# Kernel tuning notes

Measured on AMD Instinct MI355X. Metric: run time of the kernel, lower is better.

## Reference

```python
import jax, jax.numpy as jnp
import numpy as np

N = 100000
E = 500000
D = 128      # input_dim
H = 4        # heads
C = 32       # per-head out channels (H*C == D)
HID = 512    # FFN hidden
EPS = 1e-5


def _layer_norm(x, w, b):
    mu = jnp.mean(x, axis=-1, keepdims=True)
    var = jnp.mean(jnp.square(x - mu), axis=-1, keepdims=True)
    return (x - mu) * jax.lax.rsqrt(var + EPS) * w + b


def setup_inputs() -> dict:
    key = jax.random.key(0)
    ks = jax.random.split(key, 16)
    s = 1.0 / np.sqrt(D)
    inp = {
        "x": jax.random.normal(ks[0], (N, D), dtype=jnp.float32),
        "edge_index": jax.random.randint(ks[1], (2, E), 0, N, dtype=jnp.int64),
        # TransformerConv params (lin_query/key/value/skip: D -> H*C == D)
        "Wq": jax.random.normal(ks[2], (D, D), dtype=jnp.float32) * s,
        "bq": jnp.zeros((D,), jnp.float32),
        "Wk": jax.random.normal(ks[3], (D, D), dtype=jnp.float32) * s,
        "bk": jnp.zeros((D,), jnp.float32),
        "Wv": jax.random.normal(ks[4], (D, D), dtype=jnp.float32) * s,
        "bv": jnp.zeros((D,), jnp.float32),
        "Wskip": jax.random.normal(ks[5], (D, D), dtype=jnp.float32) * s,
        "bskip": jnp.zeros((D,), jnp.float32),
        # lin_out
        "Wout": jax.random.normal(ks[6], (D, D), dtype=jnp.float32) * s,
        "bout": jnp.zeros((D,), jnp.float32),
        # LayerNorms
        "ln1_w": jnp.ones((D,), jnp.float32),
        "ln1_b": jnp.zeros((D,), jnp.float32),
        "ln2_w": jnp.ones((D,), jnp.float32),
        "ln2_b": jnp.zeros((D,), jnp.float32),
        # FFN
        "W1": jax.random.normal(ks[7], (HID, D), dtype=jnp.float32) * s,
        "b1": jnp.zeros((HID,), jnp.float32),
        "W2": jax.random.normal(ks[8], (D, HID), dtype=jnp.float32) * (1.0 / np.sqrt(HID)),
        "b2": jnp.zeros((D,), jnp.float32),
    }
    return inp


def _transformer_conv(x, src, dst, Wq, bq, Wk, bk, Wv, bv, Wskip, bskip):
    # q/k/v: [N, H, C]
    q = (x @ Wq.T + bq).reshape(N, H, C)
    k = (x @ Wk.T + bk).reshape(N, H, C)
    v = (x @ Wv.T + bv).reshape(N, H, C)
    # per-edge attention logits: [E, H]
    alpha = jnp.sum(q[dst] * k[src], axis=-1) / np.sqrt(C)
    # segment softmax over incoming edges of each destination node
    m = jax.ops.segment_max(alpha, dst, num_segments=N)       # [N, H]
    e = jnp.exp(alpha - m[dst])                               # [E, H]
    z = jax.ops.segment_sum(e, dst, num_segments=N)           # [N, H]
    a = e / z[dst]                                            # [E, H]
    # weighted aggregate of values: [N, H, C]
    msg = a[:, :, None] * v[src]
    out = jax.ops.segment_sum(msg, dst, num_segments=N)
    # root/skip connection (PyG root_weight=True)
    return out.reshape(N, H * C) + x @ Wskip.T + bskip


def reference(x, Wq, bq, Wk, bk, Wv, bv, Wskip, bskip, Wout, bout,
              ln1_w, ln1_b, W1, b1, W2, b2, ln2_w, ln2_b, edge_index):
    src = edge_index[0]
    dst = edge_index[1]
    conv = _transformer_conv(x, src, dst, Wq, bq, Wk, bk, Wv, bv, Wskip, bskip)
    out1 = conv @ Wout.T + bout
    out2 = _layer_norm(out1 + x, ln1_w, ln1_b)
    h = jax.nn.relu(out2 @ W1.T + b1)
    out3 = h @ W2.T + b2
    out4 = _layer_norm(out3 + out2, ln2_w, ln2_b)
    return out4
```

## Files before the change

### kernel.cpp

```cpp
#include <hip/hip_runtime.h>

#define NN   100000
#define NE   500000
#define DD   128
#define HH   4
#define HIDD 512
#define EPSF 1e-5f

typedef __bf16 bf16x8 __attribute__((ext_vector_type(8)));
typedef float  f32x4  __attribute__((ext_vector_type(4)));

__device__ __forceinline__ unsigned short f2b(float f) {
  unsigned u = __float_as_uint(f);
  unsigned r = (u + 0x7FFFu + ((u >> 16) & 1)) >> 16;
  return (unsigned short)r;
}
__device__ __forceinline__ float b2f(unsigned short s) {
  return __uint_as_float(((unsigned)s) << 16);
}

#define GLOAD16(ldsp, gp) __builtin_amdgcn_global_load_lds(                      \
    (const __attribute__((address_space(1))) void*)(gp),                         \
    (__attribute__((address_space(3))) void*)(ldsp), 16, 0, 0)

__device__ __forceinline__ void stageW(unsigned short* lds, const unsigned short* g,
                                       int ldg, int t) {
  const int w = t >> 6, l = t & 63;
#pragma unroll
  for (int i = 0; i < 8; i++) {
    const int chunk0 = i * 256 + w * 64;
    const int chunk = chunk0 + l;
    const int row = chunk >> 4, c16 = chunk & 15;
    const int gslot = c16 ^ (row & 15);
    GLOAD16(lds + (size_t)chunk0 * 8, g + (size_t)row * ldg + gslot * 8);
  }
}

__global__ void k_cast(const float* __restrict__ src, unsigned short* __restrict__ dst, int n) {
  int i = (blockIdx.x * 256 + threadIdx.x) * 4;
  if (i >= n) return;
  float4 v = *(const float4*)&src[i];
  ushort4 o;
  o.x = f2b(v.x); o.y = f2b(v.y); o.z = f2b(v.z); o.w = f2b(v.w);
  *(ushort4*)&dst[i] = o;
}

__global__ void k_castw(const float* __restrict__ Wq, const float* __restrict__ Wk,
                        const float* __restrict__ Wv, const float* __restrict__ Wsk,
                        const float* __restrict__ Wo, const float* __restrict__ W1,
                        const float* __restrict__ W2,
                        const float* __restrict__ bq, const float* __restrict__ bk,
                        const float* __restrict__ bv, const float* __restrict__ bs,
                        unsigned short* __restrict__ Wqkvs, unsigned short* __restrict__ Wob,
                        unsigned short* __restrict__ W1b, unsigned short* __restrict__ W2b,
                        float* __restrict__ bias512) {
  int i = blockIdx.x * 256 + threadIdx.x;
  if (i < 53248) {
    int e = i * 4;
    const float* src; unsigned short* dst; int off;
    if (e < 65536) {
      int seg = e >> 14;
      const float* s4[4] = {Wq, Wk, Wv, Wsk};
      src = s4[seg]; dst = Wqkvs + (seg << 14); off = e & 16383;
    } else if (e < 81920) { src = Wo;  dst = Wob; off = e - 65536; }
    else if (e < 147456)  { src = W1;  dst = W1b; off = e - 81920; }
    else                  { src = W2;  dst = W2b; off = e - 147456; }
    float4 v = *(const float4*)&src[off];
    ushort4 o; o.x = f2b(v.x); o.y = f2b(v.y); o.z = f2b(v.z); o.w = f2b(v.w);
    *(ushort4*)&dst[off] = o;
  } else if (i < 53376) {
    int b4 = (i - 53248) * 4;
    const float* srcs[4] = {bq, bk, bv, bs};
#pragma unroll
    for (int j = 0; j < 4; j++) {
      int idx = b4 + j;
      bias512[idx] = srcs[idx >> 7][idx & 127];
    }
  }
}

__global__ void k_zero_cnt(int* __restrict__ cnt) {
  int i = blockIdx.x * 256 + threadIdx.x;
  if (i < NN) cnt[i] = 0;
}
__global__ void k_count(const int* __restrict__ ei, int* __restrict__ cnt) {
  int e = blockIdx.x * 256 + threadIdx.x;
  if (e < NE) atomicAdd(&cnt[ei[NE + e]], 1);
}
__global__ void k_scan1(const int* __restrict__ cnt, int* __restrict__ rowptr, int* __restrict__ part) {
  __shared__ int sh[256];
  int i = blockIdx.x * 256 + threadIdx.x;
  int v = (i < NN) ? cnt[i] : 0;
  sh[threadIdx.x] = v; __syncthreads();
  for (int off = 1; off < 256; off <<= 1) {
    int t = (threadIdx.x >= off) ? sh[threadIdx.x - off] : 0;
    __syncthreads();
    sh[threadIdx.x] += t;
    __syncthreads();
  }
  if (i < NN) rowptr[i] = sh[threadIdx.x] - v;
  if (threadIdx.x == 255) part[blockIdx.x] = sh[255];
}
__global__ void k_scan2(const int* __restrict__ part, int* __restrict__ partx) {
  __shared__ int sh[512];
  int t = threadIdx.x;
  int v = (t < 391) ? part[t] : 0;
  sh[t] = v; __syncthreads();
  for (int off = 1; off < 512; off <<= 1) {
    int u = (t >= off) ? sh[t - off] : 0;
    __syncthreads();
    sh[t] += u;
    __syncthreads();
  }
  partx[t] = sh[t] - v;
}
__global__ void k_scan3(int* __restrict__ rowptr, const int* __restrict__ partx, int* __restrict__ cnt) {
  int i = blockIdx.x * 256 + threadIdx.x;
  if (i < NN) {
    int r = rowptr[i] + partx[i >> 8];
    rowptr[i] = r;
    cnt[i] = r;
  }
  if (i == 0) rowptr[NN] = NE;
}
__global__ void k_scatter(const int* __restrict__ ei, int* __restrict__ cnt, int* __restrict__ csr_src) {
  int e = blockIdx.x * 256 + threadIdx.x;
  if (e >= NE) return;
  int d = ei[NE + e];
  int pos = atomicAdd(&cnt[d], 1);
  csr_src[pos] = ei[e];
}

#define LOADA(dst, Aptr, LDA_, kb)                                               \
  _Pragma("unroll") for (int ks = 0; ks < 4; ks++)                               \
    _Pragma("unroll") for (int rt = 0; rt < 2; rt++) {                           \
      const int row_ = n0 + rt * 16 + lq;                                        \
      bf16x8 zz = {};                                                            \
      dst[ks][rt] = (row_ < NN)                                                  \
          ? *(const bf16x8*)&(Aptr)[(size_t)row_ * (LDA_) + (kb) + ks * 32 + hq * 8] \
          : zz;                                                                  \
    }

__global__ __launch_bounds__(256, 2) void k_gemm_cg(const unsigned short* __restrict__ A,
                                                    const unsigned short* __restrict__ W,
                                                    const float* __restrict__ bias,
                                                    unsigned short* __restrict__ outB) {
  __shared__ __align__(16) unsigned short Ws[128 * 128];
  const int t = threadIdx.x;
  const int w = t >> 6, l = t & 63;
  const int n0 = blockIdx.x * 128 + w * 32;
  const int lq = l & 15, hq = l >> 4;

  bf16x8 af[4][2];
  LOADA(af, A, 128, 0);
#pragma unroll 1
  for (int cg = 0; cg < 4; ++cg) {
    if (cg) __syncthreads();
    stageW(Ws, W + (size_t)cg * 128 * 128, 128, t);
    __syncthreads();
    f32x4 acc[2][8] = {};
#pragma unroll
    for (int ks = 0; ks < 4; ks++) {
      bf16x8 b[8];
      const int c16 = ks * 4 + hq;
#pragma unroll
      for (int ct = 0; ct < 8; ct++) {
        const int row = ct * 16 + lq;
        b[ct] = *(const bf16x8*)&Ws[row * 128 + ((c16 ^ lq) * 8)];
      }
#pragma unroll
      for (int rt = 0; rt < 2; rt++)
#pragma unroll
        for (int ct = 0; ct < 8; ct++)
          acc[rt][ct] = __builtin_amdgcn_mfma_f32_16x16x32_bf16(b[ct], af[ks][rt], acc[rt][ct], 0, 0, 0);
    }
#pragma unroll
    for (int rt = 0; rt < 2; rt++) {
      const int row = n0 + rt * 16 + lq;
      if (row < NN) {
#pragma unroll
        for (int ct = 0; ct < 8; ct++) {
          const int col = cg * 128 + ct * 16 + hq * 4;
          const float4 bs = *(const float4*)&bias[col];
          ushort4 o;
          o.x = f2b(acc[rt][ct][0] + bs.x);
          o.y = f2b(acc[rt][ct][1] + bs.y);
          o.z = f2b(acc[rt][ct][2] + bs.z);
          o.w = f2b(acc[rt][ct][3] + bs.w);
          *(ushort4*)&outB[(size_t)row * 512 + col] = o;
        }
      }
    }
  }
}

__global__ __launch_bounds__(256, 4) void k_gemm_ln1(const unsigned short* __restrict__ A,
                                                     const unsigned short* __restrict__ W,
                                                     const float* __restrict__ bias,
                                                     const unsigned short* __restrict__ resB,
                                                     const float* __restrict__ lw,
                                                     const float* __restrict__ lb,
                                                     unsigned short* __restrict__ outB) {
  __shared__ __align__(16) unsigned short Ws[128 * 128];
  const int t = threadIdx.x;
  const int w = t >> 6, l = t & 63;
  const int n0 = blockIdx.x * 128 + w * 32;
  const int lq = l & 15, hq = l >> 4;

  bf16x8 af[4][2];
  LOADA(af, A, 512, 0);
  stageW(Ws, W, 128, t);
  __syncthreads();
  f32x4 acc[2][8] = {};
#pragma unroll
  for (int ks = 0; ks < 4; ks++) {
    bf16x8 b[8];
    const int c16 = ks * 4 + hq;
#pragma unroll
    for (int ct = 0; ct < 8; ct++) {
      const int row = ct * 16 + lq;
      b[ct] = *(const bf16x8*)&Ws[row * 128 + ((c16 ^ lq) * 8)];
    }
#pragma unroll
    for (int rt = 0; rt < 2; rt++)
#pragma unroll
      for (int ct = 0; ct < 8; ct++)
        acc[rt][ct] = __builtin_amdgcn_mfma_f32_16x16x32_bf16(b[ct], af[ks][rt], acc[rt][ct], 0, 0, 0);
  }
#pragma unroll
  for (int rt = 0; rt < 2; rt++) {
    const int row = n0 + rt * 16 + lq;
#pragma unroll
    for (int ct = 0; ct < 8; ct++) {
      const int col = ct * 16 + hq * 4;
      const float4 bs = *(const float4*)&bias[col];
      ushort4 rv = make_ushort4(0, 0, 0, 0);
      if (row < NN) rv = *(const ushort4*)&resB[(size_t)row * DD + col];
      acc[rt][ct][0] += bs.x + b2f(rv.x);
      acc[rt][ct][1] += bs.y + b2f(rv.y);
      acc[rt][ct][2] += bs.z + b2f(rv.z);
      acc[rt][ct][3] += bs.w + b2f(rv.w);
    }
    float s = 0.f;
#pragma unroll
    for (int ct = 0; ct < 8; ct++)
#pragma unroll
      for (int j = 0; j < 4; j++) s += acc[rt][ct][j];
    s += __shfl_xor(s, 16, 64); s += __shfl_xor(s, 32, 64);
    const float mu = s * (1.f / 128.f);
    float vs = 0.f;
#pragma unroll
    for (int ct = 0; ct < 8; ct++)
#pragma unroll
      for (int j = 0; j < 4; j++) { float d = acc[rt][ct][j] - mu; vs += d * d; }
    vs += __shfl_xor(vs, 16, 64); vs += __shfl_xor(vs, 32, 64);
    const float rs = rsqrtf(vs * (1.f / 128.f) + EPSF);
    if (row < NN) {
#pragma unroll
      for (int ct = 0; ct < 8; ct++) {
        const int col = ct * 16 + hq * 4;
        const float4 lw4 = *(const float4*)&lw[col];
        const float4 lb4 = *(const float4*)&lb[col];
        ushort4 o;
        o.x = f2b((acc[rt][ct][0] - mu) * rs * lw4.x + lb4.x);
        o.y = f2b((acc[rt][ct][1] - mu) * rs * lw4.y + lb4.y);
        o.z = f2b((acc[rt][ct][2] - mu) * rs * lw4.z + lb4.z);
        o.w = f2b((acc[rt][ct][3] - mu) * rs * lw4.w + lb4.w);
        *(ushort4*)&outB[(size_t)row * DD + col] = o;
      }
    }
  }
}

__global__ __launch_bounds__(256, 2) void k_ffn_fused(const unsigned short* __restrict__ A,
                                                      const unsigned short* __restrict__ W1,
                                                      const float* __restrict__ b1,
                                                      const unsigned short* __restrict__ W2,
                                                      const float* __restrict__ b2,
                                                      const float* __restrict__ lw,
                                                      const float* __restrict__ lb,
                                                      float* __restrict__ outF) {
  __shared__ __align__(16) unsigned short Ws[128 * 128];
  __shared__ __align__(16) unsigned short Hs[128 * 128];
  const int t = threadIdx.x;
  const int w = t >> 6, l = t & 63;
  const int n0 = blockIdx.x * 128 + w * 32;
  const int lq = l & 15, hq = l >> 4;
  const int lrow = w * 32;

  bf16x8 af[4][2];
  LOADA(af, A, 128, 0);

  f32x4 acc2[2][8] = {};
#pragma unroll 1
  for (int cg = 0; cg < 4; ++cg) {
    if (cg) __syncthreads();
    stageW(Ws, W1 + (size_t)cg * 128 * 128, 128, t);
    __syncthreads();
    f32x4 acc1[2][8] = {};
#pragma unroll
    for (int ks = 0; ks < 4; ks++) {
      bf16x8 b[8];
      const int c16 = ks * 4 + hq;
#pragma unroll
      for (int ct = 0; ct < 8; ct++) {
        const int row = ct * 16 + lq;
        b[ct] = *(const bf16x8*)&Ws[row * 128 + ((c16 ^ lq) * 8)];
      }
#pragma unroll
      for (int rt = 0; rt < 2; rt++)
#pragma unroll
        for (int ct = 0; ct < 8; ct++)
          acc1[rt][ct] = __builtin_amdgcn_mfma_f32_16x16x32_bf16(b[ct], af[ks][rt], acc1[rt][ct], 0, 0, 0);
    }
#pragma unroll
    for (int rt = 0; rt < 2; rt++) {
      const int row = lrow + rt * 16 + lq;
#pragma unroll
      for (int ct = 0; ct < 8; ct++) {
        const int col = ct * 16 + hq * 4;
        const float4 bs = *(const float4*)&b1[cg * 128 + col];
        ushort4 o;
        o.x = f2b(fmaxf(acc1[rt][ct][0] + bs.x, 0.f));
        o.y = f2b(fmaxf(acc1[rt][ct][1] + bs.y, 0.f));
        o.z = f2b(fmaxf(acc1[rt][ct][2] + bs.z, 0.f));
        o.w = f2b(fmaxf(acc1[rt][ct][3] + bs.w, 0.f));
        *(ushort4*)&Hs[row * 128 + (((col >> 3) ^ lq) * 8) + (col & 7)] = o;
      }
    }
    __syncthreads();
    stageW(Ws, W2 + (size_t)cg * 128, 512, t);
    __syncthreads();
#pragma unroll
    for (int ks = 0; ks < 4; ks++) {
      bf16x8 b[8];
      const int c16 = ks * 4 + hq;
#pragma unroll
      for (int ct = 0; ct < 8; ct++) {
        const int row = ct * 16 + lq;
        b[ct] = *(const bf16x8*)&Ws[row * 128 + ((c16 ^ lq) * 8)];
      }
      bf16x8 h[2];
#pragma unroll
      for (int rt = 0; rt < 2; rt++) {
        const int row = lrow + rt * 16 + lq;
        h[rt] = *(const bf16x8*)&Hs[row * 128 + (((ks * 4 + hq) ^ lq) * 8)];
      }
#pragma unroll
      for (int rt = 0; rt < 2; rt++)
#pragma unroll
        for (int ct = 0; ct < 8; ct++)
          acc2[rt][ct] = __builtin_amdgcn_mfma_f32_16x16x32_bf16(b[ct], h[rt], acc2[rt][ct], 0, 0, 0);
    }
  }

#pragma unroll
  for (int rt = 0; rt < 2; rt++) {
    const int row = n0 + rt * 16 + lq;
#pragma unroll
    for (int ct = 0; ct < 8; ct++) {
      const int col = ct * 16 + hq * 4;
      const float4 bs = *(const float4*)&b2[col];
      ushort4 rv = make_ushort4(0, 0, 0, 0);
      if (row < NN) rv = *(const ushort4*)&A[(size_t)row * DD + col];
      acc2[rt][ct][0] += bs.x + b2f(rv.x);
      acc2[rt][ct][1] += bs.y + b2f(rv.y);
      acc2[rt][ct][2] += bs.z + b2f(rv.z);
      acc2[rt][ct][3] += bs.w + b2f(rv.w);
    }
    float s = 0.f;
#pragma unroll
    for (int ct = 0; ct < 8; ct++)
#pragma unroll
      for (int j = 0; j < 4; j++) s += acc2[rt][ct][j];
    s += __shfl_xor(s, 16, 64); s += __shfl_xor(s, 32, 64);
    const float mu = s * (1.f / 128.f);
    float vs = 0.f;
#pragma unroll
    for (int ct = 0; ct < 8; ct++)
#pragma unroll
      for (int j = 0; j < 4; j++) { float d = acc2[rt][ct][j] - mu; vs += d * d; }
    vs += __shfl_xor(vs, 16, 64); vs += __shfl_xor(vs, 32, 64);
    const float rs = rsqrtf(vs * (1.f / 128.f) + EPSF);
    if (row < NN) {
#pragma unroll
      for (int ct = 0; ct < 8; ct++) {
        const int col = ct * 16 + hq * 4;
        const float4 lw4 = *(const float4*)&lw[col];
        const float4 lb4 = *(const float4*)&lb[col];
        float4 o;
        o.x = (acc2[rt][ct][0] - mu) * rs * lw4.x + lb4.x;
        o.y = (acc2[rt][ct][1] - mu) * rs * lw4.y + lb4.y;
        o.z = (acc2[rt][ct][2] - mu) * rs * lw4.z + lb4.z;
        o.w = (acc2[rt][ct][3] - mu) * rs * lw4.w + lb4.w;
        *(float4*)&outF[(size_t)row * DD + col] = o;
      }
    }
  }
}

__global__ __launch_bounds__(256) void k_attn(const int* __restrict__ csr_src,
                                              const int* __restrict__ rowptr,
                                              unsigned short* qkvsb) {
  const int l = threadIdx.x & 31;
  const int node = blockIdx.x * 8 + (threadIdx.x >> 5);
  const int row0 = rowptr[node], row1 = rowptr[node + 1];
  ushort4 qu = *(const ushort4*)&qkvsb[(size_t)node * 512 + l * 4];
  const float qx = b2f(qu.x), qy = b2f(qu.y), qz = b2f(qu.z), qw = b2f(qu.w);
  float ax = 0.f, ay = 0.f, az = 0.f, aw = 0.f, z = 0.f;
  int p = row0;
  for (; p + 2 <= row1; p += 2) {
    int s0 = csr_src[p], s1 = csr_src[p + 1];
    const unsigned short* b0 = &qkvsb[(size_t)s0 * 512];
    const unsigned short* b1 = &qkvsb[(size_t)s1 * 512];
    ushort4 k0 = *(const ushort4*)(b0 + 128 + l * 4);
    ushort4 v0 = *(const ushort4*)(b0 + 256 + l * 4);
    ushort4 k1 = *(const ushort4*)(b1 + 128 + l * 4);
    ushort4 v1 = *(const ushort4*)(b1 + 256 + l * 4);
    float d0 = qx * b2f(k0.x) + qy * b2f(k0.y) + qz * b2f(k0.z) + qw * b2f(k0.w);
    float d1 = qx * b2f(k1.x) + qy * b2f(k1.y) + qz * b2f(k1.z) + qw * b2f(k1.w);
    d0 += __shfl_xor(d0, 1, 32); d1 += __shfl_xor(d1, 1, 32);
    d0 += __shfl_xor(d0, 2, 32); d1 += __shfl_xor(d1, 2, 32);
    d0 += __shfl_xor(d0, 4, 32); d1 += __shfl_xor(d1, 4, 32);
    float e0 = __expf(d0 * 0.17677669529663687f);
    float e1 = __expf(d1 * 0.17677669529663687f);
    z += e0 + e1;
    ax += e0 * b2f(v0.x) + e1 * b2f(v1.x);
    ay += e0 * b2f(v0.y) + e1 * b2f(v1.y);
    az += e0 * b2f(v0.z) + e1 * b2f(v1.z);
    aw += e0 * b2f(v0.w) + e1 * b2f(v1.w);
  }
  if (p < row1) {
    int s = csr_src[p];
    const unsigned short* base = &qkvsb[(size_t)s * 512];
    ushort4 kr = *(const ushort4*)(base + 128 + l * 4);
    ushort4 vr = *(const ushort4*)(base + 256 + l * 4);
    float d = qx * b2f(kr.x) + qy * b2f(kr.y) + qz * b2f(kr.z) + qw * b2f(kr.w);
    d += __shfl_xor(d, 1, 32);
    d += __shfl_xor(d, 2, 32);
    d += __shfl_xor(d, 4, 32);
    float e = __expf(d * 0.17677669529663687f);
    z += e;
    ax += e * b2f(vr.x); ay += e * b2f(vr.y);
    az += e * b2f(vr.z); aw += e * b2f(vr.w);
  }
  const float rz = (z > 0.f) ? (1.f / z) : 0.f;
  ushort4 su = *(const ushort4*)&qkvsb[(size_t)node * 512 + 384 + l * 4];
  ushort4 o;
  o.x = f2b(b2f(su.x) + ax * rz);
  o.y = f2b(b2f(su.y) + ay * rz);
  o.z = f2b(b2f(su.z) + az * rz);
  o.w = f2b(b2f(su.w) + aw * rz);
  *(ushort4*)&qkvsb[(size_t)node * 512 + 384 + l * 4] = o;
}

extern "C" void kernel_launch(void* const* d_in, const int* in_sizes, int n_in,
                              void* d_out, int out_size, void* d_ws, size_t ws_size,
                              hipStream_t stream) {
  const float* x   = (const float*)d_in[0];
  const int*   ei  = (const int*)d_in[1];
  const float* Wq  = (const float*)d_in[2];
  const float* bq  = (const float*)d_in[3];
  const float* Wk  = (const float*)d_in[4];
  const float* bk  = (const float*)d_in[5];
  const float* Wv  = (const float*)d_in[6];
  const float* bv  = (const float*)d_in[7];
  const float* Wsk = (const float*)d_in[8];
  const float* bsk = (const float*)d_in[9];
  const float* Wo  = (const float*)d_in[10];
  const float* bo  = (const float*)d_in[11];
  const float* l1w = (const float*)d_in[12];
  const float* l1b = (const float*)d_in[13];
  const float* l2w = (const float*)d_in[14];
  const float* l2b = (const float*)d_in[15];
  const float* W1  = (const float*)d_in[16];
  const float* b1  = (const float*)d_in[17];
  const float* W2  = (const float*)d_in[18];
  const float* b2  = (const float*)d_in[19];

  unsigned short* wsu = (unsigned short*)d_ws;
  unsigned short* qkvsb = wsu;
  unsigned short* out2b = wsu + (size_t)NN * 512;
  unsigned short* xb    = out2b + (size_t)NN * DD;
  int* csr_src = (int*)(xb + (size_t)NN * DD);
  int* rowptr  = csr_src + NE;
  int* cnt     = rowptr + NN + 1;
  int* part    = cnt + NN;
  int* partx   = part + 512;
  size_t woff = (size_t)((partx + 512) - (int*)d_ws);
  woff = (woff + 3) & ~(size_t)3;
  unsigned short* Wqkvs = (unsigned short*)((int*)d_ws + woff);
  unsigned short* Wob   = Wqkvs + 512 * DD;
  unsigned short* W1b   = Wob + DD * DD;
  unsigned short* W2b   = W1b + (size_t)HIDD * DD;
  float* bias512        = (float*)(W2b + (size_t)DD * HIDD);

  float* outf = (float*)d_out;

  const int GX = (NN + 127) / 128;
  dim3 blk(256);

  k_cast<<<dim3(12500), blk, 0, stream>>>(x, xb, NN * DD);
  k_castw<<<dim3(209), blk, 0, stream>>>(Wq, Wk, Wv, Wsk, Wo, W1, W2, bq, bk, bv, bsk,
                                         Wqkvs, Wob, W1b, W2b, bias512);

  k_zero_cnt<<<dim3(391), blk, 0, stream>>>(cnt);
  k_count<<<dim3(1954), blk, 0, stream>>>(ei, cnt);
  k_scan1<<<dim3(391), blk, 0, stream>>>(cnt, rowptr, part);
  k_scan2<<<dim3(1), dim3(512), 0, stream>>>(part, partx);
  k_scan3<<<dim3(391), blk, 0, stream>>>(rowptr, partx, cnt);
  k_scatter<<<dim3(1954), blk, 0, stream>>>(ei, cnt, csr_src);

  k_gemm_cg<<<dim3(GX), blk, 0, stream>>>(xb, Wqkvs, bias512, qkvsb);

  k_attn<<<dim3(12500), blk, 0, stream>>>(csr_src, rowptr, qkvsb);

  k_gemm_ln1<<<dim3(GX), blk, 0, stream>>>(qkvsb + 384, Wob, bo, xb, l1w, l1b, out2b);

  k_ffn_fused<<<dim3(GX), blk, 0, stream>>>(out2b, W1b, b1, W2b, b2, l2w, l2b, outf);
}
```

Before: 271.7 us.

## Fuse x cast into QKVS GEMM and merge out-proj/LN1 with FFN kernel

Removes the separate fp32-to-bf16 cast of x by converting in the QKVS GEMM's A-load, and merges the output projection + LayerNorm1 kernel with the FFN kernel so out2 stays in LDS/registers instead of round-tripping through global memory. Blocks grow to 512 threads covering 256 rows, and weight tiles are double-buffered in LDS so the next tile's load overlaps the current MFMA phase. The residual now uses fp32 x rather than bf16 x. The cost is much more LDS per block (up to 128KB in the post kernel), which may limit occupancy and sits near the per-CU LDS limit.

```diff
diff --git a/kernel.cpp b/kernel.cpp
--- a/kernel.cpp
+++ b/kernel.cpp
@@ -9,6 +9,7 @@
 
 typedef __bf16 bf16x8 __attribute__((ext_vector_type(8)));
 typedef float  f32x4  __attribute__((ext_vector_type(4)));
+typedef unsigned short u16x8 __attribute__((ext_vector_type(8)));
 
 __device__ __forceinline__ unsigned short f2b(float f) {
   unsigned u = __float_as_uint(f);
@@ -23,26 +24,18 @@
     (const __attribute__((address_space(1))) void*)(gp),                         \
     (__attribute__((address_space(3))) void*)(ldsp), 16, 0, 0)
 
-__device__ __forceinline__ void stageW(unsigned short* lds, const unsigned short* g,
-                                       int ldg, int t) {
+template <int NT>
+__device__ __forceinline__ void stage_tile(unsigned short* lds, const unsigned short* g,
+                                           int ldg, int t) {
   const int w = t >> 6, l = t & 63;
 #pragma unroll
-  for (int i = 0; i < 8; i++) {
-    const int chunk0 = i * 256 + w * 64;
+  for (int i = 0; i < 2048 / NT; i++) {
+    const int chunk0 = i * NT + w * 64;
     const int chunk = chunk0 + l;
     const int row = chunk >> 4, c16 = chunk & 15;
     const int gslot = c16 ^ (row & 15);
     GLOAD16(lds + (size_t)chunk0 * 8, g + (size_t)row * ldg + gslot * 8);
   }
-}
-
-__global__ void k_cast(const float* __restrict__ src, unsigned short* __restrict__ dst, int n) {
-  int i = (blockIdx.x * 256 + threadIdx.x) * 4;
-  if (i >= n) return;
-  float4 v = *(const float4*)&src[i];
-  ushort4 o;
-  o.x = f2b(v.x); o.y = f2b(v.y); o.z = f2b(v.z); o.w = f2b(v.w);
-  *(ushort4*)&dst[i] = o;
 }
 
 __global__ void k_castw(const float* __restrict__ Wq, const float* __restrict__ Wk,
@@ -131,49 +124,65 @@
   csr_src[pos] = ei[e];
 }
 
-#define LOADA(dst, Aptr, LDA_, kb)                                               \
+#define LOADA(dst, Aptr, LDA_)                                                   \
   _Pragma("unroll") for (int ks = 0; ks < 4; ks++)                               \
     _Pragma("unroll") for (int rt = 0; rt < 2; rt++) {                           \
       const int row_ = n0 + rt * 16 + lq;                                        \
       bf16x8 zz = {};                                                            \
       dst[ks][rt] = (row_ < NN)                                                  \
-          ? *(const bf16x8*)&(Aptr)[(size_t)row_ * (LDA_) + (kb) + ks * 32 + hq * 8] \
+          ? *(const bf16x8*)&(Aptr)[(size_t)row_ * (LDA_) + ks * 32 + hq * 8]    \
           : zz;                                                                  \
     }
 
-__global__ __launch_bounds__(256, 2) void k_gemm_cg(const unsigned short* __restrict__ A,
-                                                    const unsigned short* __restrict__ W,
-                                                    const float* __restrict__ bias,
-                                                    unsigned short* __restrict__ outB) {
-  __shared__ __align__(16) unsigned short Ws[128 * 128];
+#define LOADA_F32(dst, Xp)                                                       \
+  _Pragma("unroll") for (int ks = 0; ks < 4; ks++)                               \
+    _Pragma("unroll") for (int rt = 0; rt < 2; rt++) {                           \
+      const int row_ = n0 + rt * 16 + lq;                                        \
+      u16x8 tmp = {};                                                            \
+      if (row_ < NN) {                                                           \
+        const float* p = (Xp) + (size_t)row_ * 128 + ks * 32 + hq * 8;           \
+        float4 f0 = *(const float4*)p, f1 = *(const float4*)(p + 4);             \
+        tmp[0]=f2b(f0.x); tmp[1]=f2b(f0.y); tmp[2]=f2b(f0.z); tmp[3]=f2b(f0.w);  \
+        tmp[4]=f2b(f1.x); tmp[5]=f2b(f1.y); tmp[6]=f2b(f1.z); tmp[7]=f2b(f1.w);  \
+      }                                                                          \
+      dst[ks][rt] = *(bf16x8*)&tmp;                                              \
+    }
+
+#define MFMA_PHASE(WS, AF, ACC)                                                  \
+  _Pragma("unroll") for (int ks = 0; ks < 4; ks++) {                             \
+    bf16x8 bb[8];                                                                \
+    const int c16_ = ks * 4 + hq;                                                \
+    _Pragma("unroll") for (int ct = 0; ct < 8; ct++) {                           \
+      const int row_ = ct * 16 + lq;                                             \
+      bb[ct] = *(const bf16x8*)&WS[row_ * 128 + ((c16_ ^ lq) * 8)];              \
+    }                                                                            \
+    _Pragma("unroll") for (int rt = 0; rt < 2; rt++)                             \
+      _Pragma("unroll") for (int ct = 0; ct < 8; ct++)                           \
+        ACC[rt][ct] = __builtin_amdgcn_mfma_f32_16x16x32_bf16(bb[ct], AF[ks][rt], ACC[rt][ct], 0, 0, 0); \
+  }
+
+__global__ __launch_bounds__(512, 2) void k_qkvs(const float* __restrict__ x,
+                                                 const unsigned short* __restrict__ W,
+                                                 const float* __restrict__ bias,
+                                                 unsigned short* __restrict__ outB) {
+  __shared__ __align__(16) unsigned short WsA[128 * 128];
+  __shared__ __align__(16) unsigned short WsB[128 * 128];
   const int t = threadIdx.x;
   const int w = t >> 6, l = t & 63;
-  const int n0 = blockIdx.x * 128 + w * 32;
+  const int n0 = blockIdx.x * 256 + w * 32;
   const int lq = l & 15, hq = l >> 4;
 
   bf16x8 af[4][2];
-  LOADA(af, A, 128, 0);
-#pragma unroll 1
+  LOADA_F32(af, x);
+  stage_tile<512>(WsA, W, 128, t);
+  __syncthreads();
+#pragma unroll
   for (int cg = 0; cg < 4; ++cg) {
-    if (cg) __syncthreads();
-    stageW(Ws, W + (size_t)cg * 128 * 128, 128, t);
-    __syncthreads();
+    unsigned short* cur = (cg & 1) ? WsB : WsA;
+    unsigned short* nxt = (cg & 1) ? WsA : WsB;
+    if (cg < 3) stage_tile<512>(nxt, W + (size_t)(cg + 1) * 128 * 128, 128, t);
     f32x4 acc[2][8] = {};
-#pragma unroll
-    for (int ks = 0; ks < 4; ks++) {
-      bf16x8 b[8];
-      const int c16 = ks * 4 + hq;
-#pragma unroll
-      for (int ct = 0; ct < 8; ct++) {
-        const int row = ct * 16 + lq;
-        b[ct] = *(const bf16x8*)&Ws[row * 128 + ((c16 ^ lq) * 8)];
-      }
-#pragma unroll
-      for (int rt = 0; rt < 2; rt++)
-#pragma unroll
-        for (int ct = 0; ct < 8; ct++)
-          acc[rt][ct] = __builtin_amdgcn_mfma_f32_16x16x32_bf16(b[ct], af[ks][rt], acc[rt][ct], 0, 0, 0);
-    }
+    MFMA_PHASE(cur, af, acc)
 #pragma unroll
     for (int rt = 0; rt < 2; rt++) {
       const int row = n0 + rt * 16 + lq;
@@ -191,55 +200,55 @@
         }
       }
     }
-  }
-}
-
-__global__ __launch_bounds__(256, 4) void k_gemm_ln1(const unsigned short* __restrict__ A,
-                                                     const unsigned short* __restrict__ W,
-                                                     const float* __restrict__ bias,
-                                                     const unsigned short* __restrict__ resB,
-                                                     const float* __restrict__ lw,
-                                                     const float* __restrict__ lb,
-                                                     unsigned short* __restrict__ outB) {
-  __shared__ __align__(16) unsigned short Ws[128 * 128];
+    if (cg < 3) __syncthreads();
+  }
+}
+
+__global__ __launch_bounds__(512, 2) void k_post(const unsigned short* __restrict__ conv,
+                                                 const float* __restrict__ x,
+                                                 const unsigned short* __restrict__ Wob,
+                                                 const float* __restrict__ bo,
+                                                 const float* __restrict__ l1w,
+                                                 const float* __restrict__ l1b,
+                                                 const unsigned short* __restrict__ W1b,
+                                                 const float* __restrict__ b1,
+                                                 const unsigned short* __restrict__ W2b,
+                                                 const float* __restrict__ b2,
+                                                 const float* __restrict__ l2w,
+                                                 const float* __restrict__ l2b,
+                                                 float* __restrict__ outF) {
+  __shared__ __align__(16) unsigned short WsA[128 * 128];
+  __shared__ __align__(16) unsigned short WsB[128 * 128];
+  __shared__ __align__(16) unsigned short Hs[256 * 128];
   const int t = threadIdx.x;
   const int w = t >> 6, l = t & 63;
-  const int n0 = blockIdx.x * 128 + w * 32;
+  const int n0 = blockIdx.x * 256 + w * 32;
   const int lq = l & 15, hq = l >> 4;
+  const int lrow = w * 32;
 
   bf16x8 af[4][2];
-  LOADA(af, A, 512, 0);
-  stageW(Ws, W, 128, t);
+  LOADA(af, conv, 512);
+  stage_tile<512>(WsA, Wob, 128, t);
   __syncthreads();
+  stage_tile<512>(WsB, W1b, 128, t);
+
   f32x4 acc[2][8] = {};
-#pragma unroll
-  for (int ks = 0; ks < 4; ks++) {
-    bf16x8 b[8];
-    const int c16 = ks * 4 + hq;
-#pragma unroll
-    for (int ct = 0; ct < 8; ct++) {
-      const int row = ct * 16 + lq;
-      b[ct] = *(const bf16x8*)&Ws[row * 128 + ((c16 ^ lq) * 8)];
-    }
-#pragma unroll
-    for (int rt = 0; rt < 2; rt++)
-#pragma unroll
-      for (int ct = 0; ct < 8; ct++)
-        acc[rt][ct] = __builtin_amdgcn_mfma_f32_16x16x32_bf16(b[ct], af[ks][rt], acc[rt][ct], 0, 0, 0);
-  }
+  MFMA_PHASE(WsA, af, acc)
+
+  ushort4 o2[2][8];
 #pragma unroll
   for (int rt = 0; rt < 2; rt++) {
     const int row = n0 + rt * 16 + lq;
 #pragma unroll
     for (int ct = 0; ct < 8; ct++) {
       const int col = ct * 16 + hq * 4;
-      const float4 bs = *(const float4*)&bias[col];
-      ushort4 rv = make_ushort4(0, 0, 0, 0);
-      if (row < NN) rv = *(const ushort4*)&resB[(size_t)row * DD + col];
-      acc[rt][ct][0] += bs.x + b2f(rv.x);
-      acc[rt][ct][1] += bs.y + b2f(rv.y);
-      acc[rt][ct][2] += bs.z + b2f(rv.z);
-      acc[rt][ct][3] += bs.w + b2f(rv.w);
+      const float4 bs = *(const float4*)&bo[col];
+      float4 rv = make_float4(0.f, 0.f, 0.f, 0.f);
+      if (row < NN) rv = *(const float4*)&x[(size_t)row * DD + col];
+      acc[rt][ct][0] += bs.x + rv.x;
+      acc[rt][ct][1] += bs.y + rv.y;
+      acc[rt][ct][2] += bs.z + rv.z;
+      acc[rt][ct][3] += bs.w + rv.w;
     }
     float s = 0.f;
 #pragma unroll
@@ -255,67 +264,39 @@
       for (int j = 0; j < 4; j++) { float d = acc[rt][ct][j] - mu; vs += d * d; }
     vs += __shfl_xor(vs, 16, 64); vs += __shfl_xor(vs, 32, 64);
     const float rs = rsqrtf(vs * (1.f / 128.f) + EPSF);
-    if (row < NN) {
-#pragma unroll
-      for (int ct = 0; ct < 8; ct++) {
-        const int col = ct * 16 + hq * 4;
-        const float4 lw4 = *(const float4*)&lw[col];
-        const float4 lb4 = *(const float4*)&lb[col];
-        ushort4 o;
-        o.x = f2b((acc[rt][ct][0] - mu) * rs * lw4.x + lb4.x);
-        o.y = f2b((acc[rt][ct][1] - mu) * rs * lw4.y + lb4.y);
-        o.z = f2b((acc[rt][ct][2] - mu) * rs * lw4.z + lb4.z);
-        o.w = f2b((acc[rt][ct][3] - mu) * rs * lw4.w + lb4.w);
-        *(ushort4*)&outB[(size_t)row * DD + col] = o;
-      }
-    }
-  }
-}
-
-__global__ __launch_bounds__(256, 2) void k_ffn_fused(const unsigned short* __restrict__ A,
-                                                      const unsigned short* __restrict__ W1,
-                                                      const float* __restrict__ b1,
-                                                      const unsigned short* __restrict__ W2,
-                                                      const float* __restrict__ b2,
-                                                      const float* __restrict__ lw,
-                                                      const float* __restrict__ lb,
-                                                      float* __restrict__ outF) {
-  __shared__ __align__(16) unsigned short Ws[128 * 128];
-  __shared__ __align__(16) unsigned short Hs[128 * 128];
-  const int t = threadIdx.x;
-  const int w = t >> 6, l = t & 63;
-  const int n0 = blockIdx.x * 128 + w * 32;
-  const int lq = l & 15, hq = l >> 4;
-  const int lrow = w * 32;
-
-  bf16x8 af[4][2];
-  LOADA(af, A, 128, 0);
+    const int hrow = lrow + rt * 16 + lq;
+#pragma unroll
+    for (int ct = 0; ct < 8; ct++) {
+      const int col = ct * 16 + hq * 4;
+      const float4 lw4 = *(const float4*)&l1w[col];
+      const float4 lb4 = *(const float4*)&l1b[col];
+      ushort4 o;
+      o.x = f2b((acc[rt][ct][0] - mu) * rs * lw4.x + lb4.x);
+      o.y = f2b((acc[rt][ct][1] - mu) * rs * lw4.y + lb4.y);
+      o.z = f2b((acc[rt][ct][2] - mu) * rs * lw4.z + lb4.z);
+      o.w = f2b((acc[rt][ct][3] - mu) * rs * lw4.w + lb4.w);
+      o2[rt][ct] = o;
+      *(ushort4*)&Hs[hrow * 128 + (((col >> 3) ^ lq) * 8) + (col & 7)] = o;
+    }
+  }
+  __syncthreads();
+
+  bf16x8 af2[4][2];
+#pragma unroll
+  for (int ks = 0; ks < 4; ks++)
+#pragma unroll
+    for (int rt = 0; rt < 2; rt++)
+      af2[ks][rt] = *(const bf16x8*)&Hs[(lrow + rt * 16 + lq) * 128 + (((ks * 4 + hq) ^ lq) * 8)];
 
   f32x4 acc2[2][8] = {};
 #pragma unroll 1
   for (int cg = 0; cg < 4; ++cg) {
-    if (cg) __syncthreads();
-    stageW(Ws, W1 + (size_t)cg * 128 * 128, 128, t);
-    __syncthreads();
+    stage_tile<512>(WsA, W2b + (size_t)cg * 128, 512, t);
     f32x4 acc1[2][8] = {};
-#pragma unroll
-    for (int ks = 0; ks < 4; ks++) {
-      bf16x8 b[8];
-      const int c16 = ks * 4 + hq;
-#pragma unroll
-      for (int ct = 0; ct < 8; ct++) {
-        const int row = ct * 16 + lq;
-        b[ct] = *(const bf16x8*)&Ws[row * 128 + ((c16 ^ lq) * 8)];
-      }
-#pragma unroll
-      for (int rt = 0; rt < 2; rt++)
-#pragma unroll
-        for (int ct = 0; ct < 8; ct++)
-          acc1[rt][ct] = __builtin_amdgcn_mfma_f32_16x16x32_bf16(b[ct], af[ks][rt], acc1[rt][ct], 0, 0, 0);
-    }
+    MFMA_PHASE(WsB, af2, acc1)
 #pragma unroll
     for (int rt = 0; rt < 2; rt++) {
-      const int row = lrow + rt * 16 + lq;
+      const int hrow = lrow + rt * 16 + lq;
 #pragma unroll
       for (int ct = 0; ct < 8; ct++) {
         const int col = ct * 16 + hq * 4;
@@ -325,33 +306,31 @@
         o.y = f2b(fmaxf(acc1[rt][ct][1] + bs.y, 0.f));
         o.z = f2b(fmaxf(acc1[rt][ct][2] + bs.z, 0.f));
         o.w = f2b(fmaxf(acc1[rt][ct][3] + bs.w, 0.f));
-        *(ushort4*)&Hs[row * 128 + (((col >> 3) ^ lq) * 8) + (col & 7)] = o;
+        *(ushort4*)&Hs[hrow * 128 + (((col >> 3) ^ lq) * 8) + (col & 7)] = o;
       }
     }
     __syncthreads();
-    stageW(Ws, W2 + (size_t)cg * 128, 512, t);
-    __syncthreads();
+    if (cg < 3) stage_tile<512>(WsB, W1b + (size_t)(cg + 1) * 128 * 128, 128, t);
 #pragma unroll
     for (int ks = 0; ks < 4; ks++) {
-      bf16x8 b[8];
-      const int c16 = ks * 4 + hq;
+      bf16x8 bb[8];
+      const int c16_ = ks * 4 + hq;
 #pragma unroll
       for (int ct = 0; ct < 8; ct++) {
-        const int row = ct * 16 + lq;
-        b[ct] = *(const bf16x8*)&Ws[row * 128 + ((c16 ^ lq) * 8)];
+        const int row_ = ct * 16 + lq;
+        bb[ct] = *(const bf16x8*)&WsA[row_ * 128 + ((c16_ ^ lq) * 8)];
       }
       bf16x8 h[2];
 #pragma unroll
-      for (int rt = 0; rt < 2; rt++) {
-        const int row = lrow + rt * 16 + lq;
-        h[rt] = *(const bf16x8*)&Hs[row * 128 + (((ks * 4 + hq) ^ lq) * 8)];
-      }
-#pragma unroll
       for (int rt = 0; rt < 2; rt++)
+        h[rt] = *(const bf16x8*)&Hs[(lrow + rt * 16 + lq) * 128 + ((c16_ ^ lq) * 8)];
+#pragma unroll
+      for (int rt = 0; rt < 2; rt++)
 #pragma unroll
         for (int ct = 0; ct < 8; ct++)
-          acc2[rt][ct] = __builtin_amdgcn_mfma_f32_16x16x32_bf16(b[ct], h[rt], acc2[rt][ct], 0, 0, 0);
-    }
+          acc2[rt][ct] = __builtin_amdgcn_mfma_f32_16x16x32_bf16(bb[ct], h[rt], acc2[rt][ct], 0, 0, 0);
+    }
+    __syncthreads();
   }
 
 #pragma unroll
@@ -361,8 +340,7 @@
     for (int ct = 0; ct < 8; ct++) {
       const int col = ct * 16 + hq * 4;
       const float4 bs = *(const float4*)&b2[col];
-      ushort4 rv = make_ushort4(0, 0, 0, 0);
-      if (row < NN) rv = *(const ushort4*)&A[(size_t)row * DD + col];
+      const ushort4 rv = o2[rt][ct];
       acc2[rt][ct][0] += bs.x + b2f(rv.x);
       acc2[rt][ct][1] += bs.y + b2f(rv.y);
       acc2[rt][ct][2] += bs.z + b2f(rv.z);
@@ -386,8 +364,8 @@
 #pragma unroll
       for (int ct = 0; ct < 8; ct++) {
         const int col = ct * 16 + hq * 4;
-        const float4 lw4 = *(const float4*)&lw[col];
-        const float4 lb4 = *(const float4*)&lb[col];
+        const float4 lw4 = *(const float4*)&l2w[col];
+        const float4 lb4 = *(const float4*)&l2b[col];
         float4 o;
         o.x = (acc2[rt][ct][0] - mu) * rs * lw4.x + lb4.x;
         o.y = (acc2[rt][ct][1] - mu) * rs * lw4.y + lb4.y;
@@ -480,9 +458,7 @@
 
   unsigned short* wsu = (unsigned short*)d_ws;
   unsigned short* qkvsb = wsu;
-  unsigned short* out2b = wsu + (size_t)NN * 512;
-  unsigned short* xb    = out2b + (size_t)NN * DD;
-  int* csr_src = (int*)(xb + (size_t)NN * DD);
+  int* csr_src = (int*)(qkvsb + (size_t)NN * 512);
   int* rowptr  = csr_src + NE;
   int* cnt     = rowptr + NN + 1;
   int* part    = cnt + NN;
@@ -497,10 +473,9 @@
 
   float* outf = (float*)d_out;
 
-  const int GX = (NN + 127) / 128;
-  dim3 blk(256);
-
-  k_cast<<<dim3(12500), blk, 0, stream>>>(x, xb, NN * DD);
+  const int GB = (NN + 255) / 256;
+  dim3 blk(256), blk5(512);
+
   k_castw<<<dim3(209), blk, 0, stream>>>(Wq, Wk, Wv, Wsk, Wo, W1, W2, bq, bk, bv, bsk,
                                          Wqkvs, Wob, W1b, W2b, bias512);
 
@@ -511,11 +486,10 @@
   k_scan3<<<dim3(391), blk, 0, stream>>>(rowptr, partx, cnt);
   k_scatter<<<dim3(1954), blk, 0, stream>>>(ei, cnt, csr_src);
 
-  k_gemm_cg<<<dim3(GX), blk, 0, stream>>>(xb, Wqkvs, bias512, qkvsb);
+  k_qkvs<<<dim3(GB), blk5, 0, stream>>>(x, Wqkvs, bias512, qkvsb);
 
   k_attn<<<dim3(12500), blk, 0, stream>>>(csr_src, rowptr, qkvsb);
 
-  k_gemm_ln1<<<dim3(GX), blk, 0, stream>>>(qkvsb + 384, Wob, bo, xb, l1w, l1b, out2b);
-
-  k_ffn_fused<<<dim3(GX), blk, 0, stream>>>(out2b, W1b, b1, W2b, b2, l2w, l2b, outf);
-}
+  k_post<<<dim3(GB), blk5, 0, stream>>>(qkvsb + 384, x, Wob, bo, l1w, l1b,
+                                        W1b, b1, W2b, b2, l2w, l2b, outf);
+}
```

New measurement: 275.3 us. About the same (+1.3%).
